# Kernel tuning notes

Measured on AMD Instinct MI355X. Metric: run time of the kernel, lower is better.

The kernel has to match this reference:

```python
import jax, jax.numpy as jnp
import numpy as np

EPS = 1e-12  # matches torch.nn.functional.normalize default eps


def _l2norm_ch(x):
    # normalize over channel axis (dim=1), x: [B, D, N]
    n = jnp.sqrt(jnp.sum(x * x, axis=1, keepdims=True))
    return x / jnp.maximum(n, EPS)


def setup_inputs() -> dict:
    key = jax.random.key(0)
    k0, k1, kq, kk, kv = jax.random.split(key, 5)
    B, D, H, W = 8, 128, 64, 64
    return {
        "vol0": jax.random.normal(k0, (B, D, H, W), dtype=jnp.float32),
        "vol1": jax.random.normal(k1, (B, D, H, W), dtype=jnp.float32),
        "Wq": jax.random.normal(kq, (D, D), dtype=jnp.float32) * 0.05,
        "Wk": jax.random.normal(kk, (D, D), dtype=jnp.float32) * 0.05,
        "Wv": jax.random.normal(kv, (D, D), dtype=jnp.float32) * 0.05,
    }


def reference(vol0, vol1, Wq, Wk, Wv):
    B, D, H, W = vol0.shape
    N = H * W
    x0 = vol0.reshape(B, D, N)
    x1 = vol1.reshape(B, D, N)

    # 1x1 convs (bias=False) == channel matmuls; residual connections enabled
    q = jnp.einsum('od,bdn->bon', Wq, x0) + x0
    k = jnp.einsum('od,bdn->bon', Wk, x1) + x1
    v0 = jnp.einsum('od,bdn->bon', Wv, x0) + x0
    v1 = jnp.einsum('od,bdn->bon', Wv, x1) + x1

    # normalise dot product: L2-normalize over channel dim
    q = _l2norm_ch(q)
    k = _l2norm_ch(k)

    # correlation volume + row softmax: cvolume[b, n, m]
    cvolume = jax.nn.softmax(jnp.einsum('bdn,bdm->bnm', q, k), axis=2)

    # warp v1 by attention: v1w[b, d, n] = sum_m v1[b, d, m] * cvolume[b, n, m]
    v1w = jnp.einsum('bdm,bnm->bdn', v1, cvolume)

    # position encoder (meshgrid with 'ij' indexing, as legacy torch.meshgrid)
    u = jnp.linspace(-1.0, 1.0, H)
    v = jnp.linspace(-1.0, 1.0, W)
    uu, vv = jnp.meshgrid(u, v, indexing='ij')
    grid = jnp.stack([uu, vv], axis=0).reshape(2, N)  # [2, N]
    pos = jnp.einsum('cm,bnm->bcn', grid, cvolume)  # [B, 2, N]

    # max-score channel: [B, 1, N]
    max_score = jnp.max(cvolume, axis=2)[:, None, :]

    agg = jnp.concatenate([v0, v1w, pos, max_score], axis=1)  # [B, 2D+3, N]
    return agg.reshape(B, 2 * D + 3, H, W)
```

## Files before the change

### kernel.cpp

```cpp
#include <hip/hip_runtime.h>
#include <hip/hip_bf16.h>

#define B_   8
#define D_   128
#define N_   4096
#define CH   259

typedef short bf8 __attribute__((ext_vector_type(8)));
typedef float f4  __attribute__((ext_vector_type(4)));

typedef unsigned int as1_u32 __attribute__((address_space(1)));
typedef unsigned int as3_u32 __attribute__((address_space(3)));

__device__ __forceinline__ void gll16(const void* g, void* l) {
    __builtin_amdgcn_global_load_lds((as1_u32*)(unsigned long long)g,
                                     (as3_u32*)(unsigned int)(unsigned long long)l,
                                     16, 0, 0);
}

__device__ __forceinline__ unsigned short f2bf(float x) {
    unsigned int u = __float_as_uint(x);
    return (unsigned short)((u + 0x7FFFu + ((u >> 16) & 1u)) >> 16);
}

__device__ __forceinline__ unsigned int cvtpk(float lo, float hi) {
    unsigned int r;
    asm("v_cvt_pk_bf16_f32 %0, %1, %2" : "=v"(r) : "v"(lo), "v"(hi));
    return r;
}

__global__ void wconv_kernel(const float* __restrict__ Wq,
                             const float* __restrict__ Wk,
                             const float* __restrict__ Wv,
                             unsigned short* __restrict__ Wb) {
    const float* src = (blockIdx.x == 0) ? Wq : (blockIdx.x == 1) ? Wk : Wv;
    unsigned short* dst = Wb + (size_t)blockIdx.x * D_ * D_;
    for (int i = threadIdx.x; i < D_ * D_; i += blockDim.x) dst[i] = f2bf(src[i]);
}

__global__ __launch_bounds__(256, 2) void proj_kernel(
    const float* __restrict__ vol0, const float* __restrict__ vol1,
    const unsigned short* __restrict__ Wb, float* __restrict__ out,
    unsigned short* __restrict__ Qp, unsigned short* __restrict__ Kh,
    unsigned short* __restrict__ V2)
{
    __shared__ __align__(16) float xs[2][D_ * 64];

    const int tid  = threadIdx.x;
    const int wave = tid >> 6, lane = tid & 63;
    const int l15  = lane & 15, lh = lane >> 4;

    const int bid = blockIdx.x;
    const int swz = (bid & 7) * 64 + (bid >> 3);
    const int b   = swz >> 6;
    const int n0  = (swz & 63) * 64;

    #pragma unroll
    for (int a = 0; a < 2; ++a) {
        const char* src = (const char*)((a ? vol1 : vol0) + (size_t)b * D_ * N_ + n0);
        char* dstb = (char*)&xs[a][0];
        #pragma unroll
        for (int i = 0; i < 8; ++i) {
            int dst16 = i * 4096 + tid * 16;
            int row = dst16 >> 8, cb = dst16 & 255;
            gll16(src + (size_t)row * (N_ * 4) + (cb ^ (((row >> 3) & 7) << 4)), dstb + dst16);
        }
    }
    __syncthreads();

    const int nrow = wave * 16 + l15;

    auto afrag = [&](const float* base, int k) -> bf8 {
        const int dbase = k * 32 + lh * 8;
        const unsigned int cb = ((unsigned int)(nrow * 4)) ^ (((unsigned int)((k * 4 + lh) & 7)) << 4);
        const float* p = base + dbase * 64 + (cb >> 2);
        union { bf8 v; unsigned int w[4]; } u;
        #pragma unroll
        for (int jj = 0; jj < 4; ++jj)
            u.w[jj] = cvtpk(p[(2 * jj) * 64], p[(2 * jj + 1) * 64]);
        return u.v;
    };

    f4 aq[8], ak[8], a0v[8], a1v[8];
    #pragma unroll
    for (int ob = 0; ob < 8; ++ob) {
        aq[ob] = (f4){0.f,0.f,0.f,0.f}; ak[ob] = (f4){0.f,0.f,0.f,0.f};
        a0v[ob] = (f4){0.f,0.f,0.f,0.f}; a1v[ob] = (f4){0.f,0.f,0.f,0.f};
    }

    const unsigned short* Wqb = Wb;
    const unsigned short* Wkb = Wb + D_ * D_;
    const unsigned short* Wvb = Wb + 2 * D_ * D_;

    for (int k = 0; k < 4; ++k) {
        bf8 x0f = afrag(&xs[0][0], k);
        bf8 x1f = afrag(&xs[1][0], k);
        #pragma unroll
        for (int ob = 0; ob < 8; ++ob) {
            const size_t woff = ((size_t)(ob * 16 + l15)) * D_ + k * 32 + lh * 8;
            bf8 wq = *(const bf8*)(Wqb + woff);
            bf8 wk = *(const bf8*)(Wkb + woff);
            bf8 wv = *(const bf8*)(Wvb + woff);
            aq[ob]  = __builtin_amdgcn_mfma_f32_16x16x32_bf16(x0f, wq, aq[ob], 0, 0, 0);
            ak[ob]  = __builtin_amdgcn_mfma_f32_16x16x32_bf16(x1f, wk, ak[ob], 0, 0, 0);
            a0v[ob] = __builtin_amdgcn_mfma_f32_16x16x32_bf16(x0f, wv, a0v[ob], 0, 0, 0);
            a1v[ob] = __builtin_amdgcn_mfma_f32_16x16x32_bf16(x1f, wv, a1v[ob], 0, 0, 0);
        }
    }

    float ssq[4] = {0.f,0.f,0.f,0.f}, ssk[4] = {0.f,0.f,0.f,0.f};
    #pragma unroll
    for (int ob = 0; ob < 8; ++ob) {
        const int o = ob * 16 + l15;
        const unsigned int okey = (((unsigned int)((o >> 3) & 7)) << 4);
        #pragma unroll
        for (int r = 0; r < 4; ++r) {
            int n = wave * 16 + lh * 4 + r;
            int ci = o * 64 + (int)(((((unsigned int)(n * 4)) ^ okey) >> 2));
            float r0 = xs[0][ci], r1 = xs[1][ci];
            aq[ob][r] += r0; ak[ob][r] += r1; a0v[ob][r] += r0; a1v[ob][r] += r1;
            ssq[r] = fmaf(aq[ob][r], aq[ob][r], ssq[r]);
            ssk[r] = fmaf(ak[ob][r], ak[ob][r], ssk[r]);
        }
    }
    #pragma unroll
    for (int off = 1; off < 16; off <<= 1)
        #pragma unroll
        for (int r = 0; r < 4; ++r) {
            ssq[r] += __shfl_xor(ssq[r], off, 64);
            ssk[r] += __shfl_xor(ssk[r], off, 64);
        }
    float rq[4], rk[4];
    #pragma unroll
    for (int r = 0; r < 4; ++r) {
        rq[r] = 1.44269504088896f / fmaxf(sqrtf(ssq[r]), 1e-12f);
        rk[r] = 1.0f / fmaxf(sqrtf(ssk[r]), 1e-12f);
    }

    const int nbase = n0 + wave * 16 + lh * 4;
    const int mh_ = nbase >> 11;
    const int tt  = (nbase & 2047) >> 5;
    const int ml  = nbase & 31;
    char* v2chunk = (char*)V2 + (((size_t)(b * 2 + mh_) * 64 + tt) * 8192) + ml * 2;

    #pragma unroll
    for (int ob = 0; ob < 8; ++ob) {
        const int o = ob * 16 + l15;
        *(f4*)(out + ((size_t)(b * CH + o)) * N_ + nbase) = a0v[ob];
        uint2 pv; pv.x = cvtpk(a1v[ob][0], a1v[ob][1]); pv.y = cvtpk(a1v[ob][2], a1v[ob][3]);
        *(uint2*)(v2chunk + (size_t)o * 64) = pv;
        uint2 pq; pq.x = cvtpk(aq[ob][0]*rq[0], aq[ob][1]*rq[1]);
        pq.y = cvtpk(aq[ob][2]*rq[2], aq[ob][3]*rq[3]);
        *(uint2*)(Qp + ((size_t)(b * D_ + o)) * N_ + nbase) = pq;
    }

    __syncthreads();
    float* chunk = &xs[0][0] + wave * 2176;
    #pragma unroll
    for (int ob = 0; ob < 8; ++ob) {
        const int o = ob * 16 + l15;
        #pragma unroll
        for (int r = 0; r < 4; ++r) chunk[o * 17 + lh * 4 + r] = ak[ob][r] * rk[r];
    }
    asm volatile("s_waitcnt lgkmcnt(0)" ::: "memory");
    __builtin_amdgcn_sched_barrier(0);
    {
        const int o0 = (lane & 15) * 8, nr = lane >> 4;
        #pragma unroll
        for (int t = 0; t < 4; ++t) {
            int nl = t * 4 + nr;
            float f[8];
            #pragma unroll
            for (int j = 0; j < 8; ++j) f[j] = chunk[(o0 + j) * 17 + nl];
            uint4 st;
            st.x = cvtpk(f[0], f[1]); st.y = cvtpk(f[2], f[3]);
            st.z = cvtpk(f[4], f[5]); st.w = cvtpk(f[6], f[7]);
            *(uint4*)(Kh + ((size_t)(b * N_ + n0 + wave * 16 + nl)) * D_ + o0) = st;
        }
    }
}

__global__ __launch_bounds__(256, 2) void attn_kernel(
    const unsigned short* __restrict__ Qp, const unsigned short* __restrict__ Kh,
    const unsigned short* __restrict__ V2, float* __restrict__ out)
{
    __shared__ __align__(16) char smem[40960];
    char* KB = smem;
    char* PB = smem + 32768;

    const int tid  = threadIdx.x;
    const int wave = tid >> 6, lane = tid & 63;
    const int l15  = lane & 15, lh = lane >> 4;
    const int mhalf = wave & 1, qpair = wave >> 1;

    const int bid = blockIdx.x;
    const int swz = (bid & 7) * 64 + (bid >> 3);
    const int b   = swz >> 6;
    const int n0  = (swz & 63) * 64;
    const int nw  = n0 + qpair * 32;

    bf8 qf[2][4];
    const unsigned short* Qb = Qp + (size_t)b * D_ * N_;
    #pragma unroll
    for (int qg = 0; qg < 2; ++qg)
        #pragma unroll
        for (int dc = 0; dc < 4; ++dc) {
            union { bf8 v; unsigned short e[8]; } u;
            #pragma unroll
            for (int j = 0; j < 8; ++j)
                u.e[j] = Qb[((size_t)(dc * 32 + lh * 8 + j)) * N_ + nw + qg * 16 + l15];
            qf[qg][dc] = u.v;
        }

    f4 acc[2][8];
    #pragma unroll
    for (int qg = 0; qg < 2; ++qg)
        #pragma unroll
        for (int dc = 0; dc < 8; ++dc) acc[qg][dc] = (f4){0.f,0.f,0.f,0.f};
    float lsum[2] = {0.f, 0.f}, pu[2] = {0.f, 0.f}, pvv[2] = {0.f, 0.f};
    float Mp[2] = {-1e30f, -1e30f};

    float vb0[8];
    #pragma unroll
    for (int s = 0; s < 2; ++s)
        #pragma unroll
        for (int r = 0; r < 4; ++r)
            vb0[s * 4 + r] = -1.f + (2.f / 63.f) * (float)(s * 16 + lh * 4 + r);

    const char* Kbytes = (const char*)(Kh + (size_t)b * N_ * D_);
    const char* Vg = (const char*)V2 + ((size_t)(b * 2 + mhalf)) * 524288
                   + l15 * 64 + lh * 16;
    char* Pw = PB + wave * 2048;

    unsigned int koffs[4];
    #pragma unroll
    for (int ii = 0; ii < 4; ++ii) {
        int r = wave * 16 + ii * 4 + (lane >> 4);
        unsigned int col = (unsigned int)((lane & 15) * 16);
        koffs[ii] = (unsigned int)(((r >> 5) * 2048 + (r & 31)) * 256)
                  + (col ^ (unsigned int)((r & 7) << 4));
    }
    auto stage = [&](int buf, int t) {
        const char* ks = Kbytes + (size_t)t * 8192;
        char* kd = KB + buf * 16384 + wave * 4096;
        #pragma unroll
        for (int ii = 0; ii < 4; ++ii) gll16(ks + koffs[ii], kd + ii * 1024);
    };

    unsigned int kcol[4];
    #pragma unroll
    for (int dc = 0; dc < 4; ++dc)
        kcol[dc] = ((unsigned int)(dc * 64 + lh * 16)) ^ ((unsigned int)((l15 & 7) << 4));
    const unsigned int pkey  = ((unsigned int)((l15 >> 1) & 3)) << 4;
    const unsigned int prow0 = (unsigned int)(l15 * 64);
    const unsigned int prow1 = (unsigned int)((16 + l15) * 64);
    const unsigned int px    = ((unsigned int)(lh * 16)) ^ pkey;

    stage(0, 0);
    __syncthreads();

    const float utb = -1.f + (2.f / 63.f) * (float)(mhalf * 32);

    for (int t = 0; t < 64; ++t) {
        const int cur = t & 1;

        const char* vp = Vg + t * 8192;
        bf8 vf[8];
        #pragma unroll
        for (int dc = 0; dc < 8; ++dc) vf[dc] = *(const bf8*)(vp + dc * 1024);

        if (t + 1 < 64) stage(cur ^ 1, t + 1);

        const char* Kc = KB + cur * 16384 + mhalf * 8192 + l15 * 256;

        f4 s00 = (f4){0.f,0.f,0.f,0.f}, s01 = (f4){0.f,0.f,0.f,0.f};
        f4 s10 = (f4){0.f,0.f,0.f,0.f}, s11 = (f4){0.f,0.f,0.f,0.f};
        __builtin_amdgcn_s_setprio(1);
        #pragma unroll
        for (int dc = 0; dc < 4; ++dc) {
            bf8 k0 = *(const bf8*)(Kc + kcol[dc]);
            bf8 k1 = *(const bf8*)(Kc + 4096 + kcol[dc]);
            s00 = __builtin_amdgcn_mfma_f32_16x16x32_bf16(k0, qf[0][dc], s00, 0, 0, 0);
            s10 = __builtin_amdgcn_mfma_f32_16x16x32_bf16(k0, qf[1][dc], s10, 0, 0, 0);
            s01 = __builtin_amdgcn_mfma_f32_16x16x32_bf16(k1, qf[0][dc], s01, 0, 0, 0);
            s11 = __builtin_amdgcn_mfma_f32_16x16x32_bf16(k1, qf[1][dc], s11, 0, 0, 0);
        }
        __builtin_amdgcn_s_setprio(0);

        const float ut   = utb + (2.f / 63.f) * (float)(t >> 1);
        const float voff = (t & 1) ? (64.f / 63.f) : 0.f;
        #pragma unroll
        for (int qg = 0; qg < 2; ++qg) {
            f4 sa = qg ? s10 : s00, sb = qg ? s11 : s01;
            float p[8];
            #pragma unroll
            for (int r = 0; r < 4; ++r) {
                p[r]     = __builtin_amdgcn_exp2f(sa[r]);
                p[4 + r] = __builtin_amdgcn_exp2f(sb[r]);
            }
            Mp[qg] = fmaxf(Mp[qg], fmaxf(fmaxf(fmaxf(sa[0], sa[1]), fmaxf(sa[2], sa[3])),
                                         fmaxf(fmaxf(sb[0], sb[1]), fmaxf(sb[2], sb[3]))));
            float ps = ((p[0]+p[1]) + (p[2]+p[3])) + ((p[4]+p[5]) + (p[6]+p[7]));
            float pvp = 0.f;
            #pragma unroll
            for (int i = 0; i < 8; ++i) pvp = fmaf(vb0[i], p[i], pvp);
            lsum[qg] += ps;
            pu[qg]  = fmaf(ut, ps, pu[qg]);
            pvv[qg] = fmaf(voff, ps, pvv[qg] + pvp);
            const unsigned int pr = qg ? prow1 : prow0;
            uint2 w0; w0.x = cvtpk(p[0], p[1]); w0.y = cvtpk(p[2], p[3]);
            uint2 w1; w1.x = cvtpk(p[4], p[5]); w1.y = cvtpk(p[6], p[7]);
            *(uint2*)(Pw + pr + (((unsigned int)(lh * 8)) ^ pkey))      = w0;
            *(uint2*)(Pw + pr + (((unsigned int)(32 + lh * 8)) ^ pkey)) = w1;
        }
        asm volatile("s_waitcnt lgkmcnt(0)" ::: "memory");
        __builtin_amdgcn_sched_barrier(0);

        bf8 pf0 = *(const bf8*)(Pw + prow0 + px);
        bf8 pf1 = *(const bf8*)(Pw + prow1 + px);
        __builtin_amdgcn_s_setprio(1);
        #pragma unroll
        for (int dc = 0; dc < 8; ++dc) {
            acc[0][dc] = __builtin_amdgcn_mfma_f32_16x16x32_bf16(pf0, vf[dc], acc[0][dc], 0, 0, 0);
            acc[1][dc] = __builtin_amdgcn_mfma_f32_16x16x32_bf16(pf1, vf[dc], acc[1][dc], 0, 0, 0);
        }
        __builtin_amdgcn_s_setprio(0);
        __syncthreads();
    }

    #pragma unroll
    for (int qg = 0; qg < 2; ++qg) {
        #pragma unroll
        for (int off = 16; off < 64; off <<= 1) {
            lsum[qg] += __shfl_xor(lsum[qg], off, 64);
            pu[qg]   += __shfl_xor(pu[qg], off, 64);
            pvv[qg]  += __shfl_xor(pvv[qg], off, 64);
            Mp[qg]    = fmaxf(Mp[qg], __shfl_xor(Mp[qg], off, 64));
        }
    }

    __syncthreads();
    float* ex  = (float*)smem;
    float* stt = (float*)(smem + 34816);
    if (lane < 16) {
        #pragma unroll
        for (int qg = 0; qg < 2; ++qg) {
            float* s = stt + ((wave * 2 + qg) * 16 + l15) * 4;
            s[0] = lsum[qg]; s[1] = pu[qg]; s[2] = pvv[qg]; s[3] = Mp[qg];
        }
    }
    #pragma unroll
    for (int qg = 0; qg < 2; ++qg)
        #pragma unroll
        for (int j = 0; j < 4; ++j) {
            float* e = ex + (((wave * 2 + qg) * 4 + j) * 16 + lh * 4) * 17 + l15;
            if (mhalf == 0) {
                #pragma unroll
                for (int r = 0; r < 4; ++r) e[r * 17] = acc[qg][4 + j][r];
            } else {
                #pragma unroll
                for (int r = 0; r < 4; ++r) e[r * 17] = acc[qg][j][r];
            }
        }
    __syncthreads();

    const int pw_ = wave ^ 1;
    float rl[2], PUm[2], PVm[2], Mm[2];
    #pragma unroll
    for (int qg = 0; qg < 2; ++qg) {
        const float* s = stt + ((pw_ * 2 + qg) * 16 + l15) * 4;
        float Lm = lsum[qg] + s[0];
        PUm[qg] = pu[qg]  + s[1];
        PVm[qg] = pvv[qg] + s[2];
        Mm[qg]  = fmaxf(Mp[qg], s[3]);
        rl[qg]  = __builtin_amdgcn_rcpf(Lm);
    }

    #pragma unroll
    for (int qg = 0; qg < 2; ++qg) {
        float rlr[4];
        #pragma unroll
        for (int r = 0; r < 4; ++r)
            rlr[r] = __shfl(rl[qg], (lane & 48) + lh * 4 + r, 64);
        #pragma unroll
        for (int j = 0; j < 4; ++j) {
            const float* e = ex + (((pw_ * 2 + qg) * 4 + j) * 16 + lh * 4) * 17 + l15;
            f4 v;
            if (mhalf == 0) {
                #pragma unroll
                for (int r = 0; r < 4; ++r) v[r] = (acc[qg][j][r] + e[r * 17]) * rlr[r];
            } else {
                #pragma unroll
                for (int r = 0; r < 4; ++r) v[r] = (acc[qg][4 + j][r] + e[r * 17]) * rlr[r];
            }
            const int och = 128 + (mhalf * 4 + j) * 16 + l15;
            *(f4*)(out + ((size_t)(b * CH + och)) * N_ + nw + qg * 16 + lh * 4) = v;
        }
    }
    if (mhalf == 0 && lh == 0) {
        #pragma unroll
        for (int qg = 0; qg < 2; ++qg) {
            const int gn = nw + qg * 16 + l15;
            out[((size_t)(b * CH + 256)) * N_ + gn] = PUm[qg] * rl[qg];
            out[((size_t)(b * CH + 257)) * N_ + gn] = PVm[qg] * rl[qg];
            out[((size_t)(b * CH + 258)) * N_ + gn] =
                __builtin_amdgcn_exp2f(Mm[qg]) * rl[qg];
        }
    }
}

extern "C" void kernel_launch(void* const* d_in, const int* in_sizes, int n_in,
                              void* d_out, int out_size, void* d_ws, size_t ws_size,
                              hipStream_t stream) {
    const float* vol0 = (const float*)d_in[0];
    const float* vol1 = (const float*)d_in[1];
    const float* Wq   = (const float*)d_in[2];
    const float* Wk   = (const float*)d_in[3];
    const float* Wv   = (const float*)d_in[4];
    float* out = (float*)d_out;

    char* ws = (char*)d_ws;
    const size_t QP_BYTES  = (size_t)B_ * D_ * N_ * 2;
    const size_t KH_BYTES  = (size_t)B_ * N_ * D_ * 2;
    const size_t V2_BYTES  = (size_t)B_ * D_ * N_ * 2;
    unsigned short* Qp  = (unsigned short*)(ws);
    unsigned short* Kh  = (unsigned short*)(ws + QP_BYTES);
    unsigned short* V2  = (unsigned short*)(ws + QP_BYTES + KH_BYTES);
    unsigned short* Wb  = (unsigned short*)(ws + QP_BYTES + KH_BYTES + V2_BYTES);

    hipLaunchKernelGGL(wconv_kernel, dim3(3), dim3(256), 0, stream, Wq, Wk, Wv, Wb);
    hipLaunchKernelGGL(proj_kernel, dim3(512), dim3(256), 0, stream,
                       vol0, vol1, Wb, out, Qp, Kh, V2);
    hipLaunchKernelGGL(attn_kernel, dim3(512), dim3(256), 0, stream,
                       Qp, Kh, V2, out);
}
```

Before: 142.6 us.

## Double query tile per block and stage V through LDS alongside K

The attention kernel now uses 512-thread blocks covering 128 queries instead of 64, halving the grid and sharing each staged K/V tile across twice as many query waves. V is no longer loaded by each wave directly from global memory into registers. It is copied into a double-buffered, swizzled LDS region with async global-to-LDS loads, with half the waves staging K and half staging V. The V2 layout in the projection kernel is rewritten to match the new chunk indexing. LDS use per block doubles to 80KB, which may limit occupancy with two blocks per CU, and the 256-block grid may underfill the GPU's CUs.

```diff
diff --git a/kernel.cpp b/kernel.cpp
--- a/kernel.cpp
+++ b/kernel.cpp
@@ -138,10 +138,8 @@
     }
 
     const int nbase = n0 + wave * 16 + lh * 4;
-    const int mh_ = nbase >> 11;
-    const int tt  = (nbase & 2047) >> 5;
-    const int ml  = nbase & 31;
-    char* v2chunk = (char*)V2 + (((size_t)(b * 2 + mh_) * 64 + tt) * 8192) + ml * 2;
+    char* v2chunk = (char*)V2 + ((size_t)(b * 128 + (nbase >> 5))) * 8192
+                  + (nbase & 31) * 2;
 
     #pragma unroll
     for (int ob = 0; ob < 8; ++ob) {
@@ -180,24 +178,25 @@
     }
 }
 
-__global__ __launch_bounds__(256, 2) void attn_kernel(
+__global__ __launch_bounds__(512, 2) void attn_kernel(
     const unsigned short* __restrict__ Qp, const unsigned short* __restrict__ Kh,
     const unsigned short* __restrict__ V2, float* __restrict__ out)
 {
-    __shared__ __align__(16) char smem[40960];
+    __shared__ __align__(16) char smem[81920];
     char* KB = smem;
-    char* PB = smem + 32768;
+    char* VB = smem + 32768;
+    char* PB = smem + 65536;
 
     const int tid  = threadIdx.x;
     const int wave = tid >> 6, lane = tid & 63;
     const int l15  = lane & 15, lh = lane >> 4;
-    const int mhalf = wave & 1, qpair = wave >> 1;
+    const int mhalf = wave & 1, qquad = wave >> 1;
 
     const int bid = blockIdx.x;
-    const int swz = (bid & 7) * 64 + (bid >> 3);
-    const int b   = swz >> 6;
-    const int n0  = (swz & 63) * 64;
-    const int nw  = n0 + qpair * 32;
+    const int swz = (bid & 7) * 32 + (bid >> 3);
+    const int b   = swz >> 5;
+    const int n0  = (swz & 31) * 128;
+    const int nw  = n0 + qquad * 32;
 
     bf8 qf[2][4];
     const unsigned short* Qb = Qp + (size_t)b * D_ * N_;
@@ -228,23 +227,37 @@
             vb0[s * 4 + r] = -1.f + (2.f / 63.f) * (float)(s * 16 + lh * 4 + r);
 
     const char* Kbytes = (const char*)(Kh + (size_t)b * N_ * D_);
-    const char* Vg = (const char*)V2 + ((size_t)(b * 2 + mhalf)) * 524288
-                   + l15 * 64 + lh * 16;
+    const char* Vbytes = (const char*)V2 + ((size_t)b * 128) * 8192;
     char* Pw = PB + wave * 2048;
 
-    unsigned int koffs[4];
+    const int sK = (wave < 4);
+    const int smh = sK ? (wave >> 1) : ((wave - 4) >> 1);
+    const int spt = sK ? (wave & 1) : ((wave - 4) & 1);
+    unsigned int soffs[4];
     #pragma unroll
     for (int ii = 0; ii < 4; ++ii) {
-        int r = wave * 16 + ii * 4 + (lane >> 4);
-        unsigned int col = (unsigned int)((lane & 15) * 16);
-        koffs[ii] = (unsigned int)(((r >> 5) * 2048 + (r & 31)) * 256)
-                  + (col ^ (unsigned int)((r & 7) << 4));
+        if (sK) {
+            int rr = spt * 16 + ii * 4 + (lane >> 4);
+            unsigned int col = (unsigned int)((lane & 15) * 16);
+            soffs[ii] = (unsigned int)(rr * 256) + (col ^ (unsigned int)((rr & 7) << 4));
+        } else {
+            int vr = spt * 64 + ii * 16 + (lane >> 2);
+            unsigned int mc = (unsigned int)((lane & 3) * 16);
+            soffs[ii] = (unsigned int)(vr * 64) + (mc ^ (unsigned int)(((vr >> 1) & 3) << 4));
+        }
     }
     auto stage = [&](int buf, int t) {
-        const char* ks = Kbytes + (size_t)t * 8192;
-        char* kd = KB + buf * 16384 + wave * 4096;
-        #pragma unroll
-        for (int ii = 0; ii < 4; ++ii) gll16(ks + koffs[ii], kd + ii * 1024);
+        if (sK) {
+            const char* ks = Kbytes + (size_t)smh * 524288 + (size_t)t * 8192;
+            char* kd = KB + buf * 16384 + smh * 8192 + spt * 4096;
+            #pragma unroll
+            for (int ii = 0; ii < 4; ++ii) gll16(ks + soffs[ii], kd + ii * 1024);
+        } else {
+            const char* vs = Vbytes + ((size_t)(smh * 64 + t)) * 8192;
+            char* vd = VB + buf * 16384 + smh * 8192 + spt * 4096;
+            #pragma unroll
+            for (int ii = 0; ii < 4; ++ii) gll16(vs + soffs[ii], vd + ii * 1024);
+        }
     };
 
     unsigned int kcol[4];
@@ -255,23 +268,18 @@
     const unsigned int prow0 = (unsigned int)(l15 * 64);
     const unsigned int prow1 = (unsigned int)((16 + l15) * 64);
     const unsigned int px    = ((unsigned int)(lh * 16)) ^ pkey;
+    const unsigned int vxx   = ((unsigned int)(lh * 16)) ^ pkey;
 
     stage(0, 0);
     __syncthreads();
 
-    const float utb = -1.f + (2.f / 63.f) * (float)(mhalf * 32);
-
     for (int t = 0; t < 64; ++t) {
         const int cur = t & 1;
-
-        const char* vp = Vg + t * 8192;
-        bf8 vf[8];
-        #pragma unroll
-        for (int dc = 0; dc < 8; ++dc) vf[dc] = *(const bf8*)(vp + dc * 1024);
-
         if (t + 1 < 64) stage(cur ^ 1, t + 1);
 
         const char* Kc = KB + cur * 16384 + mhalf * 8192 + l15 * 256;
+        const char* Vc = VB + cur * 16384 + mhalf * 8192 + l15 * 64 + vxx;
+        const int c = mhalf * 64 + t;
 
         f4 s00 = (f4){0.f,0.f,0.f,0.f}, s01 = (f4){0.f,0.f,0.f,0.f};
         f4 s10 = (f4){0.f,0.f,0.f,0.f}, s11 = (f4){0.f,0.f,0.f,0.f};
@@ -287,8 +295,8 @@
         }
         __builtin_amdgcn_s_setprio(0);
 
-        const float ut   = utb + (2.f / 63.f) * (float)(t >> 1);
-        const float voff = (t & 1) ? (64.f / 63.f) : 0.f;
+        const float ut   = -1.f + (2.f / 63.f) * (float)(c >> 1);
+        const float voff = (c & 1) ? (64.f / 63.f) : 0.f;
         #pragma unroll
         for (int qg = 0; qg < 2; ++qg) {
             f4 sa = qg ? s10 : s00, sb = qg ? s11 : s01;
@@ -321,8 +329,9 @@
         __builtin_amdgcn_s_setprio(1);
         #pragma unroll
         for (int dc = 0; dc < 8; ++dc) {
-            acc[0][dc] = __builtin_amdgcn_mfma_f32_16x16x32_bf16(pf0, vf[dc], acc[0][dc], 0, 0, 0);
-            acc[1][dc] = __builtin_amdgcn_mfma_f32_16x16x32_bf16(pf1, vf[dc], acc[1][dc], 0, 0, 0);
+            bf8 vfd = *(const bf8*)(Vc + dc * 1024);
+            acc[0][dc] = __builtin_amdgcn_mfma_f32_16x16x32_bf16(pf0, vfd, acc[0][dc], 0, 0, 0);
+            acc[1][dc] = __builtin_amdgcn_mfma_f32_16x16x32_bf16(pf1, vfd, acc[1][dc], 0, 0, 0);
         }
         __builtin_amdgcn_s_setprio(0);
         __syncthreads();
@@ -341,7 +350,7 @@
 
     __syncthreads();
     float* ex  = (float*)smem;
-    float* stt = (float*)(smem + 34816);
+    float* stt = (float*)(smem + 69632);
     if (lane < 16) {
         #pragma unroll
         for (int qg = 0; qg < 2; ++qg) {
@@ -431,6 +440,6 @@
     hipLaunchKernelGGL(wconv_kernel, dim3(3), dim3(256), 0, stream, Wq, Wk, Wv, Wb);
     hipLaunchKernelGGL(proj_kernel, dim3(512), dim3(256), 0, stream,
                        vol0, vol1, Wb, out, Qp, Kh, V2);
-    hipLaunchKernelGGL(attn_kernel, dim3(512), dim3(256), 0, stream,
+    hipLaunchKernelGGL(attn_kernel, dim3(256), dim3(512), 0, stream,
                        Qp, Kh, V2, out);
 }
```

Result: no change. 141.0 us (-1.1%).
